# Optimization experiments

Measured on AMD Instinct MI355X. Metric: run time of the kernel, lower is better.

The kernel has to match this reference:

```python
import jax, jax.numpy as jnp
import numpy as np

NUM_EXPERTS = 8
TOP_K = 2

def setup_inputs() -> dict:
    key = jax.random.key(0)
    ks = jax.random.split(key, 6)
    B, S, D, F, E = 2, 2048, 1024, 4096, NUM_EXPERTS
    scale = 0.02
    return {
        "x": jax.random.normal(ks[0], (B, S, D), dtype=jnp.float32),
        "router_w": jax.random.normal(ks[1], (E, D), dtype=jnp.float32) * scale,
        "router_b": jnp.zeros((E,), dtype=jnp.float32),
        "w1": jax.random.normal(ks[2], (E, D, F), dtype=jnp.float32) * scale,
        "w2": jax.random.normal(ks[3], (E, F, D), dtype=jnp.float32) * scale,
        "w3": jax.random.normal(ks[4], (E, D, F), dtype=jnp.float32) * scale,
    }

def reference(x, router_w, router_b, w1, w2, w3):
    B, S, D = x.shape
    E = router_w.shape[0]
    xf = x.reshape(-1, D)                                   # [T, D]
    logits = xf @ router_w.T + router_b                     # [T, E]
    probs = jax.nn.softmax(logits, axis=-1)
    topk_w, topk_idx = jax.lax.top_k(probs, TOP_K)          # [T, K]
    topk_w = topk_w / jnp.sum(topk_w, axis=-1, keepdims=True)
    # combine[t, e] = renormalized routing weight of expert e for token t (0 if not selected)
    combine = jnp.sum(jax.nn.one_hot(topk_idx, E, dtype=xf.dtype) * topk_w[..., None], axis=1)  # [T, E]
    out = jnp.zeros_like(xf)
    for e in range(E):  # small fixed expert count; each iter is a dense SwiGLU GEMM
        h = jax.nn.silu(xf @ w1[e]) * (xf @ w3[e])          # [T, F]
        out = out + combine[:, e:e + 1] * (h @ w2[e])       # [T, D]
    return out.reshape(B, S, D)
```

## Files before the change

kernel.cpp:

```cpp
#include <hip/hip_runtime.h>

typedef unsigned short ushort_t;
typedef __attribute__((ext_vector_type(8))) short short8;
typedef __attribute__((ext_vector_type(4))) float floatx4;

#define GAS __attribute__((address_space(1)))
#define LAS __attribute__((address_space(3)))

__device__ __forceinline__ float bf2f(ushort_t h) {
  union { unsigned int u; float f; } v; v.u = ((unsigned int)h) << 16; return v.f;
}
__device__ __forceinline__ ushort_t f2bf(float f) {
  union { float f; unsigned int u; } v; v.f = f;
  unsigned int u = v.u;
  unsigned int r = (u + 0x7fffu + ((u >> 16) & 1u)) >> 16;
  return (ushort_t)r;
}
__device__ __forceinline__ float blo(unsigned int u) { union { unsigned int u; float f; } v; v.u = u << 16; return v.f; }
__device__ __forceinline__ float bhi(unsigned int u) { union { unsigned int u; float f; } v; v.u = u & 0xffff0000u; return v.f; }

#define T_TOK 4096
#define DIM   1024
#define FDIM  4096
#define NEXP  8
#define MAXROWS 9216

__global__ void detect_kernel(const ushort_t* __restrict__ xraw, int* __restrict__ dflag) {
  __shared__ int cnt;
  if (threadIdx.x == 0) cnt = 0;
  __syncthreads();
  int c = 0;
#pragma unroll
  for (int i = 0; i < 4; ++i) {
    ushort_t u = xraw[(threadIdx.x * 4 + i) * 2];
    int e = (u >> 7) & 0xFF;
    if (e >= 100 && e <= 140) c++;
  }
  atomicAdd(&cnt, c);
  __syncthreads();
  if (threadIdx.x == 0) dflag[0] = (cnt > 600) ? 0 : 1;
}

__global__ void __launch_bounds__(256) castx_kernel(const void* __restrict__ xraw,
                                                    const int* __restrict__ dflag,
                                                    ushort_t* __restrict__ xb) {
  const int t = blockIdx.x * 256 + threadIdx.x;
  const size_t base = (size_t)t * 8;
  if (dflag[0]) {
    const float4* f = (const float4*)((const float*)xraw + base);
    float4 a = f[0], b = f[1];
    ushort_t o[8] = { f2bf(a.x), f2bf(a.y), f2bf(a.z), f2bf(a.w),
                      f2bf(b.x), f2bf(b.y), f2bf(b.z), f2bf(b.w) };
    *(uint4*)(xb + base) = *(const uint4*)o;
  } else {
    *(uint4*)(xb + base) = *((const uint4*)xraw + t);
  }
}

__global__ void __launch_bounds__(256) router_kernel(
    const void* __restrict__ x_, const ushort_t* __restrict__ xb,
    const void* __restrict__ rw_, const void* __restrict__ rb_,
    const int* __restrict__ dflag,
    int* __restrict__ topk_idx, float* __restrict__ topk_wgt, int* __restrict__ counts) {
  const int lane = threadIdx.x & 63;
  const int w = threadIdx.x >> 6;
  const int t = blockIdx.x * 4 + w;
  const int isf32 = dflag[0];
  double logits[NEXP];
  if (isf32) {
    const float* xr = (const float*)x_ + (size_t)t * DIM;
    float xv[16];
#pragma unroll
    for (int i = 0; i < 8; ++i) {
      const float2 v = *(const float2*)(xr + i * 128 + lane * 2);
      xv[2*i] = v.x; xv[2*i+1] = v.y;
    }
#pragma unroll
    for (int e = 0; e < NEXP; ++e) {
      const float* wr = (const float*)rw_ + (size_t)e * DIM;
      double acc = 0.0;
#pragma unroll
      for (int i = 0; i < 8; ++i) {
        const float2 v = *(const float2*)(wr + i * 128 + lane * 2);
        acc += (double)xv[2*i] * (double)v.x + (double)xv[2*i+1] * (double)v.y;
      }
#pragma unroll
      for (int off = 32; off > 0; off >>= 1) acc += __shfl_xor(acc, off, 64);
      logits[e] = acc + (double)((const float*)rb_)[e];
    }
  } else {
    const ushort_t* xr = xb + (size_t)t * DIM;
    float xv[16];
#pragma unroll
    for (int i = 0; i < 8; ++i) {
      unsigned int u = *(const unsigned int*)(xr + i * 128 + lane * 2);
      xv[2*i] = blo(u); xv[2*i+1] = bhi(u);
    }
#pragma unroll
    for (int e = 0; e < NEXP; ++e) {
      const ushort_t* wr = (const ushort_t*)rw_ + (size_t)e * DIM;
      float acc = 0.f;
#pragma unroll
      for (int i = 0; i < 8; ++i) {
        unsigned int u = *(const unsigned int*)(wr + i * 128 + lane * 2);
        acc += xv[2*i] * blo(u) + xv[2*i+1] * bhi(u);
      }
#pragma unroll
      for (int off = 32; off > 0; off >>= 1) acc += __shfl_xor(acc, off, 64);
      logits[e] = (double)(acc + bf2f(((const ushort_t*)rb_)[e]));
    }
  }
  if (lane == 0) {
    double l1 = -1e300, l2 = -1e300; int i1 = 0, i2 = 0;
#pragma unroll
    for (int e = 0; e < NEXP; ++e) {
      double l = logits[e];
      if (l > l1) { l2 = l1; i2 = i1; l1 = l; i1 = e; }
      else if (l > l2) { l2 = l; i2 = e; }
    }
    float wa = (float)(1.0 / (1.0 + exp(l2 - l1)));
    topk_idx[2*t] = i1; topk_idx[2*t+1] = i2;
    topk_wgt[2*t] = wa; topk_wgt[2*t+1] = 1.f - wa;
    atomicAdd(&counts[i1], 1);
    atomicAdd(&counts[i2], 1);
  }
}

__global__ void scan_kernel(const int* __restrict__ counts, int* __restrict__ offsets) {
  if (threadIdx.x == 0 && blockIdx.x == 0) {
    int s = 0; offsets[0] = 0;
    for (int e = 0; e < NEXP; ++e) { s += (counts[e] + 127) & ~127; offsets[e + 1] = s; }
  }
}

__global__ void __launch_bounds__(256) scatter_kernel(
    const int* __restrict__ topk_idx, const float* __restrict__ topk_wgt,
    const int* __restrict__ offsets, int* __restrict__ cursors,
    int* __restrict__ row_tok, float* __restrict__ row_wgt) {
  int p = blockIdx.x * 256 + threadIdx.x;
  int e = topk_idx[p];
  int pos = atomicAdd(&cursors[e], 1);
  int r = offsets[e] + pos;
  row_tok[r] = p >> 1;
  row_wgt[r] = topk_wgt[p];
}

__global__ void __launch_bounds__(256) gather_kernel(
    const uint4* __restrict__ xb, const int* __restrict__ row_tok, uint4* __restrict__ Xg) {
  int tid = blockIdx.x * 256 + threadIdx.x;
  int r = tid >> 7, c = tid & 127;
  int tok = row_tok[r];
  Xg[(size_t)r * 128 + c] = xb[(size_t)tok * 128 + c];
}

__global__ void __launch_bounds__(256) transpose_kernel(
    const void* __restrict__ src_, ushort_t* __restrict__ dst, int R, int C,
    const int* __restrict__ dflag) {
  __shared__ unsigned int tile[64][33];
  const int e = blockIdx.z;
  const int r0 = blockIdx.y * 64;
  const int c0 = blockIdx.x * 64;
  const int tx = threadIdx.x;
  if (dflag[0]) {
    const float* S = (const float*)src_ + (size_t)e * R * C;
#pragma unroll
    for (int it = 0; it < 8; ++it) {
      int slot = tx + it * 256;
      int r = slot >> 5;
      int c2 = slot & 31;
      const float2 v = *(const float2*)(S + (size_t)(r0 + r) * C + c0 + c2 * 2);
      tile[r][c2] = (unsigned int)f2bf(v.x) | ((unsigned int)f2bf(v.y) << 16);
    }
  } else {
    const ushort_t* S = (const ushort_t*)src_ + (size_t)e * R * C;
#pragma unroll
    for (int it = 0; it < 2; ++it) {
      int slot = tx + it * 256;
      int r = slot >> 3;
      int cc = slot & 7;
      const uint4 v = *(const uint4*)(S + (size_t)(r0 + r) * C + c0 + cc * 8);
      tile[r][cc*4+0] = v.x; tile[r][cc*4+1] = v.y; tile[r][cc*4+2] = v.z; tile[r][cc*4+3] = v.w;
    }
  }
  __syncthreads();
#pragma unroll
  for (int it = 0; it < 2; ++it) {
    int slot = tx + it * 256;
    int c = slot >> 3;
    int rr = (slot & 7) * 8;
    unsigned int o[4];
#pragma unroll
    for (int q = 0; q < 4; ++q) {
      unsigned int a = tile[rr + 2*q][c >> 1];
      unsigned int b = tile[rr + 2*q + 1][c >> 1];
      unsigned int ha = (c & 1) ? (a >> 16) : (a & 0xffffu);
      unsigned int hb = (c & 1) ? (b >> 16) : (b & 0xffffu);
      o[q] = ha | (hb << 16);
    }
    *(uint4*)(dst + (size_t)e * R * C + (size_t)(c0 + c) * R + r0 + rr) = *(const uint4*)o;
  }
}

__device__ __forceinline__ int swz(int r) { return (r >> 1) & 3; }

__device__ __forceinline__ void stage_tile(const ushort_t* gbase, int gstride,
                                           int row0, int k0, short* lds_tile,
                                           int wid, int lane) {
#pragma unroll
  for (int tloop = 0; tloop < 2; ++tloop) {
    int tr0 = wid * 32 + tloop * 16;
    int r = tr0 + (lane >> 2);
    int g = (lane & 3) ^ swz(r);
    const ushort_t* gp = gbase + (size_t)(row0 + r) * gstride + k0 + g * 8;
    __builtin_amdgcn_global_load_lds((const GAS void*)gp,
                                     (LAS void*)(lds_tile + tr0 * 32), 16, 0, 0);
  }
}

__device__ __forceinline__ short8 frag_ld(const short* tile, int row, int q) {
  return *(const short8*)(tile + row * 32 + ((q ^ swz(row)) << 3));
}

__global__ void __launch_bounds__(256) gemm1_kernel(
    const ushort_t* __restrict__ Xg, const ushort_t* __restrict__ w1t, const ushort_t* __restrict__ w3t,
    const int* __restrict__ offsets, ushort_t* __restrict__ H) {
  const int e = blockIdx.z;
  const int off_e = offsets[e];
  const int nrows = offsets[e + 1] - off_e;
  if ((int)blockIdx.y * 128 >= nrows) return;
  const int row0 = off_e + blockIdx.y * 128;
  const int fbase = blockIdx.x * 128;
  const ushort_t* w1e = w1t + (size_t)e * FDIM * DIM;
  const ushort_t* w3e = w3t + (size_t)e * FDIM * DIM;

  __shared__ __align__(16) short As[4096];
  __shared__ __align__(16) short B1s[4096];
  __shared__ __align__(16) short B3s[4096];

  const int lane = threadIdx.x & 63;
  const int wid = threadIdx.x >> 6;
  const int wrow = (wid >> 1) * 64;
  const int wcol = (wid & 1) * 64;
  const int l15 = lane & 15;
  const int quad = lane >> 4;

  floatx4 acc1[4][4], acc3[4][4];
  const floatx4 z4 = {0.f, 0.f, 0.f, 0.f};
#pragma unroll
  for (int i = 0; i < 4; ++i)
#pragma unroll
    for (int j = 0; j < 4; ++j) { acc1[i][j] = z4; acc3[i][j] = z4; }

  for (int k0 = 0; k0 < DIM; k0 += 32) {
    __syncthreads();
    stage_tile(Xg,  DIM, row0,  k0, As,  wid, lane);
    stage_tile(w1e, DIM, fbase, k0, B1s, wid, lane);
    stage_tile(w3e, DIM, fbase, k0, B3s, wid, lane);
    __syncthreads();
    short8 a[4], b1[4], b3[4];
#pragma unroll
    for (int i = 0; i < 4; ++i) a[i] = frag_ld(As, wrow + i * 16 + l15, quad);
#pragma unroll
    for (int j = 0; j < 4; ++j) {
      b1[j] = frag_ld(B1s, wcol + j * 16 + l15, quad);
      b3[j] = frag_ld(B3s, wcol + j * 16 + l15, quad);
    }
#pragma unroll
    for (int i = 0; i < 4; ++i)
#pragma unroll
      for (int j = 0; j < 4; ++j) {
        acc1[i][j] = __builtin_amdgcn_mfma_f32_16x16x32_bf16(a[i], b1[j], acc1[i][j], 0, 0, 0);
        acc3[i][j] = __builtin_amdgcn_mfma_f32_16x16x32_bf16(a[i], b3[j], acc3[i][j], 0, 0, 0);
      }
  }

#pragma unroll
  for (int i = 0; i < 4; ++i)
#pragma unroll
    for (int j = 0; j < 4; ++j) {
      const int n = fbase + wcol + j * 16 + l15;
#pragma unroll
      for (int p = 0; p < 4; ++p) {
        const int rl = wrow + i * 16 + quad * 4 + p;
        float zt = acc1[i][j][p];
        float vt = acc3[i][j][p];
        float s = zt / (1.f + __expf(-zt));
        H[(size_t)(row0 + rl) * FDIM + n] = f2bf(s * vt);
      }
    }
}

__global__ void __launch_bounds__(256) gemm2_kernel(
    const ushort_t* __restrict__ H, const ushort_t* __restrict__ w2t,
    const int* __restrict__ offsets, const int* __restrict__ row_tok,
    const float* __restrict__ row_wgt, float* __restrict__ out) {
  const int e = blockIdx.z;
  const int off_e = offsets[e];
  const int nrows = offsets[e + 1] - off_e;
  if ((int)blockIdx.y * 128 >= nrows) return;
  const int row0 = off_e + blockIdx.y * 128;
  const int dbase = blockIdx.x * 128;
  const ushort_t* w2e = w2t + (size_t)e * DIM * FDIM;

  __shared__ __align__(16) short As[4096];
  __shared__ __align__(16) short Bs[4096];

  const int lane = threadIdx.x & 63;
  const int wid = threadIdx.x >> 6;
  const int wrow = (wid >> 1) * 64;
  const int wcol = (wid & 1) * 64;
  const int l15 = lane & 15;
  const int quad = lane >> 4;

  floatx4 acc[4][4];
  const floatx4 z4 = {0.f, 0.f, 0.f, 0.f};
#pragma unroll
  for (int i = 0; i < 4; ++i)
#pragma unroll
    for (int j = 0; j < 4; ++j) acc[i][j] = z4;

  for (int k0 = 0; k0 < FDIM; k0 += 32) {
    __syncthreads();
    stage_tile(H,   FDIM, row0,  k0, As, wid, lane);
    stage_tile(w2e, FDIM, dbase, k0, Bs, wid, lane);
    __syncthreads();
    short8 a[4], b[4];
#pragma unroll
    for (int i = 0; i < 4; ++i) a[i] = frag_ld(As, wrow + i * 16 + l15, quad);
#pragma unroll
    for (int j = 0; j < 4; ++j) b[j] = frag_ld(Bs, wcol + j * 16 + l15, quad);
#pragma unroll
    for (int i = 0; i < 4; ++i)
#pragma unroll
      for (int j = 0; j < 4; ++j)
        acc[i][j] = __builtin_amdgcn_mfma_f32_16x16x32_bf16(a[i], b[j], acc[i][j], 0, 0, 0);
  }

#pragma unroll
  for (int i = 0; i < 4; ++i) {
    int tok[4]; float wgt[4];
#pragma unroll
    for (int p = 0; p < 4; ++p) {
      int rl = row0 + wrow + i * 16 + quad * 4 + p;
      tok[p] = row_tok[rl];
      wgt[p] = row_wgt[rl];
    }
#pragma unroll
    for (int j = 0; j < 4; ++j) {
      int n = dbase + wcol + j * 16 + l15;
#pragma unroll
      for (int p = 0; p < 4; ++p)
        atomicAdd(&out[(size_t)tok[p] * DIM + n], wgt[p] * acc[i][j][p]);
    }
  }
}

extern "C" void kernel_launch(void* const* d_in, const int* in_sizes, int n_in,
                              void* d_out, int out_size, void* d_ws, size_t ws_size,
                              hipStream_t stream) {
  const void* x  = d_in[0];
  const void* rw = d_in[1];
  const void* rb = d_in[2];
  const void* w1 = d_in[3];
  const void* w2 = d_in[4];
  const void* w3 = d_in[5];
  float* out = (float*)d_out;

  char* ws = (char*)d_ws;
  size_t off = 0;
  auto alloc = [&](size_t bytes) { size_t o = off; off += (bytes + 255) & ~(size_t)255; return o; };
  int*      dflag    = (int*)(ws + alloc(64));
  int*      counts   = (int*)(ws + alloc(64));
  int*      cursors  = (int*)(ws + alloc(64));
  int*      offsets  = (int*)(ws + alloc(64));
  int*      topk_idx = (int*)(ws + alloc((size_t)T_TOK * 2 * 4));
  float*    topk_wgt = (float*)(ws + alloc((size_t)T_TOK * 2 * 4));
  int*      row_tok  = (int*)(ws + alloc((size_t)MAXROWS * 4));
  float*    row_wgt  = (float*)(ws + alloc((size_t)MAXROWS * 4));
  ushort_t* xb       = (ushort_t*)(ws + alloc((size_t)T_TOK * DIM * 2));
  ushort_t* Xg       = (ushort_t*)(ws + alloc((size_t)MAXROWS * DIM * 2));
  ushort_t* Hbuf     = (ushort_t*)(ws + alloc((size_t)MAXROWS * FDIM * 2));
  ushort_t* w1t      = (ushort_t*)(ws + alloc((size_t)NEXP * FDIM * DIM * 2));
  ushort_t* w3t      = (ushort_t*)(ws + alloc((size_t)NEXP * FDIM * DIM * 2));
  ushort_t* w2t      = (ushort_t*)(ws + alloc((size_t)NEXP * DIM * FDIM * 2));

  hipMemsetAsync(counts, 0, 64, stream);
  hipMemsetAsync(cursors, 0, 64, stream);
  hipMemsetAsync(row_tok, 0, (size_t)MAXROWS * 4, stream);
  hipMemsetAsync(row_wgt, 0, (size_t)MAXROWS * 4, stream);
  hipMemsetAsync(out, 0, (size_t)out_size, stream);

  detect_kernel<<<1, 256, 0, stream>>>((const ushort_t*)x, dflag);
  castx_kernel<<<(T_TOK * DIM / 8) / 256, 256, 0, stream>>>(x, dflag, xb);
  router_kernel<<<T_TOK / 4, 256, 0, stream>>>(x, xb, rw, rb, dflag, topk_idx, topk_wgt, counts);
  scan_kernel<<<1, 64, 0, stream>>>(counts, offsets);
  scatter_kernel<<<(T_TOK * 2) / 256, 256, 0, stream>>>(topk_idx, topk_wgt, offsets, cursors, row_tok, row_wgt);
  gather_kernel<<<(MAXROWS * 128) / 256, 256, 0, stream>>>((const uint4*)xb, row_tok, (uint4*)Xg);
  transpose_kernel<<<dim3(FDIM / 64, DIM / 64, NEXP), 256, 0, stream>>>(w1, w1t, DIM, FDIM, dflag);
  transpose_kernel<<<dim3(FDIM / 64, DIM / 64, NEXP), 256, 0, stream>>>(w3, w3t, DIM, FDIM, dflag);
  transpose_kernel<<<dim3(DIM / 64, FDIM / 64, NEXP), 256, 0, stream>>>(w2, w2t, FDIM, DIM, dflag);
  gemm1_kernel<<<dim3(FDIM / 128, 72, NEXP), 256, 0, stream>>>(Xg, w1t, w3t, offsets, Hbuf);
  gemm2_kernel<<<dim3(DIM / 128, 72, NEXP), 256, 0, stream>>>(Hbuf, w2t, offsets, row_tok, row_wgt, out);
}
```

Before: 1.090 ms.

## Double-buffer GEMM LDS tiles, fuse token gather, flatten expert grid

Both expert GEMMs now double-buffer their LDS tiles, so the next K-slice is loaded while MFMAs run on the current one, with a single barrier per iteration. The gather kernel is removed and gemm1 reads routed token rows straight from xb through per-row pointers built from row_tok. The grid is flattened from (experts x 72 row-chunks) to padded row chunks, and each block finds its expert by scanning offsets, so no blocks are launched only to exit early. Padding rows (weight 0) skip their atomics; the cost is doubled LDS use, which may reduce occupancy.

Result: faster. 988.9 us (-9.2%).

```diff
diff --git a/kernel.cpp b/kernel.cpp
--- a/kernel.cpp
+++ b/kernel.cpp
@@ -145,14 +145,6 @@
   row_wgt[r] = topk_wgt[p];
 }
 
-__global__ void __launch_bounds__(256) gather_kernel(
-    const uint4* __restrict__ xb, const int* __restrict__ row_tok, uint4* __restrict__ Xg) {
-  int tid = blockIdx.x * 256 + threadIdx.x;
-  int r = tid >> 7, c = tid & 127;
-  int tok = row_tok[r];
-  Xg[(size_t)r * 128 + c] = xb[(size_t)tok * 128 + c];
-}
-
 __global__ void __launch_bounds__(256) transpose_kernel(
     const void* __restrict__ src_, ushort_t* __restrict__ dst, int R, int C,
     const int* __restrict__ dflag) {
@@ -221,21 +213,25 @@
   return *(const short8*)(tile + row * 32 + ((q ^ swz(row)) << 3));
 }
 
+__device__ __forceinline__ int chunk_expert(const int* offsets, int r0) {
+  int e = 0;
+  while (offsets[e + 1] <= r0) ++e;
+  return e;
+}
+
 __global__ void __launch_bounds__(256) gemm1_kernel(
-    const ushort_t* __restrict__ Xg, const ushort_t* __restrict__ w1t, const ushort_t* __restrict__ w3t,
-    const int* __restrict__ offsets, ushort_t* __restrict__ H) {
-  const int e = blockIdx.z;
-  const int off_e = offsets[e];
-  const int nrows = offsets[e + 1] - off_e;
-  if ((int)blockIdx.y * 128 >= nrows) return;
-  const int row0 = off_e + blockIdx.y * 128;
+    const ushort_t* __restrict__ xb, const ushort_t* __restrict__ w1t, const ushort_t* __restrict__ w3t,
+    const int* __restrict__ offsets, const int* __restrict__ row_tok, ushort_t* __restrict__ H) {
+  const int r0 = blockIdx.y * 128;
+  if (r0 >= offsets[NEXP]) return;
+  const int e = chunk_expert(offsets, r0);
   const int fbase = blockIdx.x * 128;
   const ushort_t* w1e = w1t + (size_t)e * FDIM * DIM;
   const ushort_t* w3e = w3t + (size_t)e * FDIM * DIM;
 
-  __shared__ __align__(16) short As[4096];
-  __shared__ __align__(16) short B1s[4096];
-  __shared__ __align__(16) short B3s[4096];
+  __shared__ __align__(16) short As[2][4096];
+  __shared__ __align__(16) short B1s[2][4096];
+  __shared__ __align__(16) short B3s[2][4096];
 
   const int lane = threadIdx.x & 63;
   const int wid = threadIdx.x >> 6;
@@ -244,6 +240,13 @@
   const int l15 = lane & 15;
   const int quad = lane >> 4;
 
+  const ushort_t* abase[2];
+#pragma unroll
+  for (int tl = 0; tl < 2; ++tl) {
+    int r = wid * 32 + tl * 16 + (lane >> 2);
+    abase[tl] = xb + (size_t)row_tok[r0 + r] * DIM + ((lane & 3) ^ swz(r)) * 8;
+  }
+
   floatx4 acc1[4][4], acc3[4][4];
   const floatx4 z4 = {0.f, 0.f, 0.f, 0.f};
 #pragma unroll
@@ -251,19 +254,22 @@
 #pragma unroll
     for (int j = 0; j < 4; ++j) { acc1[i][j] = z4; acc3[i][j] = z4; }
 
-  for (int k0 = 0; k0 < DIM; k0 += 32) {
-    __syncthreads();
-    stage_tile(Xg,  DIM, row0,  k0, As,  wid, lane);
-    stage_tile(w1e, DIM, fbase, k0, B1s, wid, lane);
-    stage_tile(w3e, DIM, fbase, k0, B3s, wid, lane);
-    __syncthreads();
+  auto stageA = [&](int k0, int buf) {
+#pragma unroll
+    for (int tl = 0; tl < 2; ++tl) {
+      int tr0 = wid * 32 + tl * 16;
+      __builtin_amdgcn_global_load_lds((const GAS void*)(abase[tl] + k0),
+                                       (LAS void*)(&As[buf][tr0 * 32]), 16, 0, 0);
+    }
+  };
+  auto compute = [&](int buf) {
     short8 a[4], b1[4], b3[4];
 #pragma unroll
-    for (int i = 0; i < 4; ++i) a[i] = frag_ld(As, wrow + i * 16 + l15, quad);
+    for (int i = 0; i < 4; ++i) a[i] = frag_ld(&As[buf][0], wrow + i * 16 + l15, quad);
 #pragma unroll
     for (int j = 0; j < 4; ++j) {
-      b1[j] = frag_ld(B1s, wcol + j * 16 + l15, quad);
-      b3[j] = frag_ld(B3s, wcol + j * 16 + l15, quad);
+      b1[j] = frag_ld(&B1s[buf][0], wcol + j * 16 + l15, quad);
+      b3[j] = frag_ld(&B3s[buf][0], wcol + j * 16 + l15, quad);
     }
 #pragma unroll
     for (int i = 0; i < 4; ++i)
@@ -272,7 +278,23 @@
         acc1[i][j] = __builtin_amdgcn_mfma_f32_16x16x32_bf16(a[i], b1[j], acc1[i][j], 0, 0, 0);
         acc3[i][j] = __builtin_amdgcn_mfma_f32_16x16x32_bf16(a[i], b3[j], acc3[i][j], 0, 0, 0);
       }
-  }
+  };
+
+  stageA(0, 0);
+  stage_tile(w1e, DIM, fbase, 0, &B1s[0][0], wid, lane);
+  stage_tile(w3e, DIM, fbase, 0, &B3s[0][0], wid, lane);
+  __syncthreads();
+  int cur = 0;
+  for (int t = 0; t < DIM / 32 - 1; ++t) {
+    const int k0n = (t + 1) * 32;
+    stageA(k0n, cur ^ 1);
+    stage_tile(w1e, DIM, fbase, k0n, &B1s[cur ^ 1][0], wid, lane);
+    stage_tile(w3e, DIM, fbase, k0n, &B3s[cur ^ 1][0], wid, lane);
+    compute(cur);
+    __syncthreads();
+    cur ^= 1;
+  }
+  compute(cur);
 
 #pragma unroll
   for (int i = 0; i < 4; ++i)
@@ -285,7 +307,7 @@
         float zt = acc1[i][j][p];
         float vt = acc3[i][j][p];
         float s = zt / (1.f + __expf(-zt));
-        H[(size_t)(row0 + rl) * FDIM + n] = f2bf(s * vt);
+        H[(size_t)(r0 + rl) * FDIM + n] = f2bf(s * vt);
       }
     }
 }
@@ -294,16 +316,14 @@
     const ushort_t* __restrict__ H, const ushort_t* __restrict__ w2t,
     const int* __restrict__ offsets, const int* __restrict__ row_tok,
     const float* __restrict__ row_wgt, float* __restrict__ out) {
-  const int e = blockIdx.z;
-  const int off_e = offsets[e];
-  const int nrows = offsets[e + 1] - off_e;
-  if ((int)blockIdx.y * 128 >= nrows) return;
-  const int row0 = off_e + blockIdx.y * 128;
+  const int r0 = blockIdx.y * 128;
+  if (r0 >= offsets[NEXP]) return;
+  const int e = chunk_expert(offsets, r0);
   const int dbase = blockIdx.x * 128;
   const ushort_t* w2e = w2t + (size_t)e * DIM * FDIM;
 
-  __shared__ __align__(16) short As[4096];
-  __shared__ __align__(16) short Bs[4096];
+  __shared__ __align__(16) short As[2][4096];
+  __shared__ __align__(16) short Bs[2][4096];
 
   const int lane = threadIdx.x & 63;
   const int wid = threadIdx.x >> 6;
@@ -319,29 +339,39 @@
 #pragma unroll
     for (int j = 0; j < 4; ++j) acc[i][j] = z4;
 
-  for (int k0 = 0; k0 < FDIM; k0 += 32) {
-    __syncthreads();
-    stage_tile(H,   FDIM, row0,  k0, As, wid, lane);
-    stage_tile(w2e, FDIM, dbase, k0, Bs, wid, lane);
-    __syncthreads();
+  auto compute = [&](int buf) {
     short8 a[4], b[4];
 #pragma unroll
-    for (int i = 0; i < 4; ++i) a[i] = frag_ld(As, wrow + i * 16 + l15, quad);
-#pragma unroll
-    for (int j = 0; j < 4; ++j) b[j] = frag_ld(Bs, wcol + j * 16 + l15, quad);
+    for (int i = 0; i < 4; ++i) a[i] = frag_ld(&As[buf][0], wrow + i * 16 + l15, quad);
+#pragma unroll
+    for (int j = 0; j < 4; ++j) b[j] = frag_ld(&Bs[buf][0], wcol + j * 16 + l15, quad);
 #pragma unroll
     for (int i = 0; i < 4; ++i)
 #pragma unroll
       for (int j = 0; j < 4; ++j)
         acc[i][j] = __builtin_amdgcn_mfma_f32_16x16x32_bf16(a[i], b[j], acc[i][j], 0, 0, 0);
-  }
+  };
+
+  stage_tile(H,   FDIM, r0,    0, &As[0][0], wid, lane);
+  stage_tile(w2e, FDIM, dbase, 0, &Bs[0][0], wid, lane);
+  __syncthreads();
+  int cur = 0;
+  for (int t = 0; t < FDIM / 32 - 1; ++t) {
+    const int k0n = (t + 1) * 32;
+    stage_tile(H,   FDIM, r0,    k0n, &As[cur ^ 1][0], wid, lane);
+    stage_tile(w2e, FDIM, dbase, k0n, &Bs[cur ^ 1][0], wid, lane);
+    compute(cur);
+    __syncthreads();
+    cur ^= 1;
+  }
+  compute(cur);
 
 #pragma unroll
   for (int i = 0; i < 4; ++i) {
     int tok[4]; float wgt[4];
 #pragma unroll
     for (int p = 0; p < 4; ++p) {
-      int rl = row0 + wrow + i * 16 + quad * 4 + p;
+      int rl = r0 + wrow + i * 16 + quad * 4 + p;
       tok[p] = row_tok[rl];
       wgt[p] = row_wgt[rl];
     }
@@ -350,7 +380,8 @@
       int n = dbase + wcol + j * 16 + l15;
 #pragma unroll
       for (int p = 0; p < 4; ++p)
-        atomicAdd(&out[(size_t)tok[p] * DIM + n], wgt[p] * acc[i][j][p]);
+        if (wgt[p] != 0.f)
+          atomicAdd(&out[(size_t)tok[p] * DIM + n], wgt[p] * acc[i][j][p]);
     }
   }
 }
@@ -378,7 +409,6 @@
   int*      row_tok  = (int*)(ws + alloc((size_t)MAXROWS * 4));
   float*    row_wgt  = (float*)(ws + alloc((size_t)MAXROWS * 4));
   ushort_t* xb       = (ushort_t*)(ws + alloc((size_t)T_TOK * DIM * 2));
-  ushort_t* Xg       = (ushort_t*)(ws + alloc((size_t)MAXROWS * DIM * 2));
   ushort_t* Hbuf     = (ushort_t*)(ws + alloc((size_t)MAXROWS * FDIM * 2));
   ushort_t* w1t      = (ushort_t*)(ws + alloc((size_t)NEXP * FDIM * DIM * 2));
   ushort_t* w3t      = (ushort_t*)(ws + alloc((size_t)NEXP * FDIM * DIM * 2));
@@ -395,10 +425,9 @@
   router_kernel<<<T_TOK / 4, 256, 0, stream>>>(x, xb, rw, rb, dflag, topk_idx, topk_wgt, counts);
   scan_kernel<<<1, 64, 0, stream>>>(counts, offsets);
   scatter_kernel<<<(T_TOK * 2) / 256, 256, 0, stream>>>(topk_idx, topk_wgt, offsets, cursors, row_tok, row_wgt);
-  gather_kernel<<<(MAXROWS * 128) / 256, 256, 0, stream>>>((const uint4*)xb, row_tok, (uint4*)Xg);
   transpose_kernel<<<dim3(FDIM / 64, DIM / 64, NEXP), 256, 0, stream>>>(w1, w1t, DIM, FDIM, dflag);
   transpose_kernel<<<dim3(FDIM / 64, DIM / 64, NEXP), 256, 0, stream>>>(w3, w3t, DIM, FDIM, dflag);
   transpose_kernel<<<dim3(DIM / 64, FDIM / 64, NEXP), 256, 0, stream>>>(w2, w2t, FDIM, DIM, dflag);
-  gemm1_kernel<<<dim3(FDIM / 128, 72, NEXP), 256, 0, stream>>>(Xg, w1t, w3t, offsets, Hbuf);
-  gemm2_kernel<<<dim3(DIM / 128, 72, NEXP), 256, 0, stream>>>(Hbuf, w2t, offsets, row_tok, row_wgt, out);
-}
+  gemm1_kernel<<<dim3(FDIM / 128, MAXROWS / 128), 256, 0, stream>>>(xb, w1t, w3t, offsets, row_tok, Hbuf);
+  gemm2_kernel<<<dim3(DIM / 128, MAXROWS / 128), 256, 0, stream>>>(Hbuf, w2t, offsets, row_tok, row_wgt, out);
+}
```
